# Kernel tuning notes

Hardware: AMD Instinct MI355X
Metric: run time of the kernel (lower is better)

The kernel has to match this reference:

```python
import jax, jax.numpy as jnp
import numpy as np

B, S, H, NH = 16, 1024, 512, 8
DH = H // NH
EPS = 1e-12
COV_MIN = 1e-24


def _split_heads(x):
    b, s, _ = x.shape
    return x.reshape(b, s, NH, DH).transpose(0, 2, 1, 3)  # [B,NH,S,DH]


def _merge_heads(x):
    b, nh, s, dh = x.shape
    return x.transpose(0, 2, 1, 3).reshape(b, s, nh * dh)


def _layernorm(x, w, b):
    u = jnp.mean(x, -1, keepdims=True)
    s = jnp.mean((x - u) ** 2, -1, keepdims=True)
    return w * ((x - u) / jnp.sqrt(s + EPS)) + b


def _wasserstein(mq, cq, mk, ck):
    # mean part: ||mq_i - mk_j||^2 via matmul expansion
    ret = (-2.0 * jnp.einsum('bhid,bhjd->bhij', mq, mk)
           + jnp.sum(mq ** 2, -1)[..., :, None]
           + jnp.sum(mk ** 2, -1)[..., None, :])
    sq_cq = jnp.sqrt(jnp.clip(cq, COV_MIN))
    sq_ck = jnp.sqrt(jnp.clip(ck, COV_MIN))
    cov_ret = (-2.0 * jnp.einsum('bhid,bhjd->bhij', sq_cq, sq_ck)
               + jnp.sum(cq, -1)[..., :, None]
               + jnp.sum(ck, -1)[..., None, :])
    return ret + cov_ret


def setup_inputs() -> dict:
    key = jax.random.key(0)
    ks = jax.random.split(key, 16)
    d = {
        'x_mean': jax.random.normal(ks[0], (B, S, H), jnp.float32),
        'x_resp_mean': jax.random.normal(ks[1], (B, S, H), jnp.float32),
        'x_cov': jax.random.normal(ks[2], (B, S, H), jnp.float32),
        'x_resp_cov': jax.random.normal(ks[3], (B, S, H), jnp.float32),
    }
    causal = jnp.tril(jnp.ones((S, S), bool))
    d['attn_mask'] = jnp.where(causal, 0.0, -1e4).astype(jnp.float32)[None, None]
    names = ['mq', 'mk', 'mv', 'cq', 'ck', 'cv', 'md', 'cd']
    for i, n in enumerate(names):
        d[n + '_w'] = jax.random.normal(ks[4 + i], (H, H), jnp.float32) * 0.02
        d[n + '_b'] = jnp.zeros((H,), jnp.float32)
    d['ln_w'] = jnp.ones((H,), jnp.float32)
    d['ln_b'] = jnp.zeros((H,), jnp.float32)
    return d


def reference(x_mean, x_resp_mean, x_cov, x_resp_cov, attn_mask,
              mq_w, mq_b, mk_w, mk_b, mv_w, mv_b,
              cq_w, cq_b, ck_w, ck_b, cv_w, cv_b,
              md_w, md_b, cd_w, cd_b, ln_w, ln_b):
    mq = _split_heads(x_mean @ mq_w + mq_b)
    mk = _split_heads(x_mean @ mk_w + mk_b)
    mv = _split_heads(x_resp_mean @ mv_w + mv_b)
    cq = _split_heads(jax.nn.elu(x_cov @ cq_w + cq_b) + 1.0)
    ck = _split_heads(jax.nn.elu(x_cov @ ck_w + ck_b) + 1.0)
    cv = _split_heads(jax.nn.elu(x_resp_cov @ cv_w + cv_b) + 1.0)

    scores = -_wasserstein(mq, cq, mk, ck) / np.sqrt(DH).astype(np.float32)
    scores = scores + attn_mask
    probs = jax.nn.softmax(scores, axis=-1)  # [B,NH,S,S]
    # zero_pad=True: zero out the first query row
    probs = probs.at[:, :, 0, :].set(0.0)

    mean_ctx = _merge_heads(jnp.einsum('bhij,bhjd->bhid', probs, mv))
    cov_ctx = _merge_heads(jnp.einsum('bhij,bhjd->bhid', probs ** 2, cv))

    mean_h = _layernorm(mean_ctx @ md_w + md_b + x_mean, ln_w, ln_b)
    cov_h = _layernorm(cov_ctx @ cd_w + cd_b + x_cov, ln_w, ln_b)
    return mean_h, cov_h, probs
```

## Files before the change

kernel.cpp:

```cpp
#include <hip/hip_runtime.h>
#include <math.h>

#define SLEN 1024
#define NH 8
#define DH 64
#define HDIM 512
#define BATCH 16
#define NROWS (BATCH * SLEN)
#define BHN (BATCH * NH)
#define BHROWS (BHN * SLEN)

typedef short bf16x8 __attribute__((ext_vector_type(8)));
typedef unsigned short u16x8 __attribute__((ext_vector_type(8)));
typedef float f32x4 __attribute__((ext_vector_type(4)));

__device__ __forceinline__ unsigned short f2bf(float f) {
    unsigned u = __float_as_uint(f);
    u += 0x7fffu + ((u >> 16) & 1u);
    return (unsigned short)(u >> 16);
}
__device__ __forceinline__ float bf2f(unsigned short h) {
    return __uint_as_float(((unsigned)h) << 16);
}

struct Args {
    const float *xm, *xrm, *xc, *xrc;
    const float *w[8], *bias[8];
    const float *ln_w, *ln_b;
    unsigned short *xbf, *wt;
    float *sums;
    unsigned short *qcat, *kcat, *vcat, *vcat_t, *ctxm, *ctxc;
    float *out_m, *out_c, *probs;
};

__global__ void __launch_bounds__(256) cvt_inputs_k(Args P) {
    const int which = blockIdx.y;
    const float *s = which == 0 ? P.xm : which == 1 ? P.xrm : which == 2 ? P.xc : P.xrc;
    unsigned short *d = P.xbf + (size_t)which * 8388608;
    const long long i = ((long long)blockIdx.x * 256 + threadIdx.x) * 8;
    if (i >= 8388608) return;
    float4 a = *(const float4 *)(s + i);
    float4 b = *(const float4 *)(s + i + 4);
    u16x8 o;
    o[0] = f2bf(a.x); o[1] = f2bf(a.y); o[2] = f2bf(a.z); o[3] = f2bf(a.w);
    o[4] = f2bf(b.x); o[5] = f2bf(b.y); o[6] = f2bf(b.z); o[7] = f2bf(b.w);
    *(u16x8 *)(d + i) = o;
}

__global__ void __launch_bounds__(256) wtrans_k(Args P) {
    const int op = blockIdx.y;
    const float *W = P.w[op];
    unsigned short *WT = P.wt + (size_t)op * 262144;
    const int kt = blockIdx.x >> 3, nt = blockIdx.x & 7;
    __shared__ float Ws[64][65];
    const int t = threadIdx.x;
#pragma unroll
    for (int it = 0; it < 4; ++it) {
        int g = t + 256 * it;
        int k = g >> 4, n4 = (g & 15) * 4;
        float4 v = *(const float4 *)(W + (size_t)(kt * 64 + k) * 512 + nt * 64 + n4);
        Ws[k][n4] = v.x; Ws[k][n4 + 1] = v.y; Ws[k][n4 + 2] = v.z; Ws[k][n4 + 3] = v.w;
    }
    __syncthreads();
#pragma unroll
    for (int it = 0; it < 2; ++it) {
        int g = t + 256 * it;
        int n = g >> 3, kg = (g & 7) * 8;
        u16x8 o;
#pragma unroll
        for (int e = 0; e < 8; ++e) o[e] = f2bf(Ws[kg + e][n]);
        *(u16x8 *)(WT + (size_t)(nt * 64 + n) * 512 + kt * 64 + kg) = o;
    }
}

__global__ void __launch_bounds__(256) mgemm0_k(Args P) {
    const int op = blockIdx.z;
    const int srcidx[6] = {0, 0, 1, 2, 2, 3};
    const unsigned short *Abf = P.xbf + (size_t)srcidx[op] * 8388608;
    const unsigned short *WT = P.wt + (size_t)op * 262144;
    const float *bias = P.bias[op];
    unsigned short *dstb; int doff, act;
    switch (op) {
        case 0: dstb = P.qcat; doff = 0;  act = 0; break;
        case 1: dstb = P.kcat; doff = 0;  act = 0; break;
        case 2: dstb = P.vcat; doff = 0;  act = 0; break;
        case 3: dstb = P.qcat; doff = 64; act = 1; break;
        case 4: dstb = P.kcat; doff = 64; act = 1; break;
        default:dstb = P.vcat; doff = 64; act = 2; break;
    }
    const int lin = blockIdx.y * 4 + blockIdx.x;
    const int xcd = lin & 7, idx = lin >> 3;
    const int m0 = (xcd * 16 + (idx >> 2)) * 128;
    const int n0 = (idx & 3) * 128;

    __shared__ unsigned short As[128][64];
    __shared__ unsigned short Bs[128][64];
    const int t = threadIdx.x;
    const int wid = t >> 6, lane = t & 63;
    const int wm = wid >> 1, wn = wid & 1;
    const int l16 = lane & 15, lq = lane >> 4;

    f32x4 acc[4][4];
#pragma unroll
    for (int i = 0; i < 4; ++i)
#pragma unroll
        for (int j = 0; j < 4; ++j) acc[i][j] = (f32x4)(0.f);

    for (int k0 = 0; k0 < 512; k0 += 64) {
        __syncthreads();
#pragma unroll
        for (int it = 0; it < 4; ++it) {
            int g = t + 256 * it;
            int r = g >> 3, cg = g & 7;
            bf16x8 av = *(const bf16x8 *)(Abf + (size_t)(m0 + r) * 512 + k0 + cg * 8);
            *(bf16x8 *)&As[r][(cg ^ (r & 7)) * 8] = av;
            bf16x8 bv = *(const bf16x8 *)(WT + (size_t)(n0 + r) * 512 + k0 + cg * 8);
            *(bf16x8 *)&Bs[r][(cg ^ (r & 7)) * 8] = bv;
        }
        __syncthreads();
#pragma unroll
        for (int kk = 0; kk < 2; ++kk) {
            bf16x8 a[4], b[4];
#pragma unroll
            for (int mf = 0; mf < 4; ++mf) {
                int r = wm * 64 + mf * 16 + l16;
                int cg = kk * 4 + lq;
                a[mf] = *(const bf16x8 *)&As[r][(cg ^ (r & 7)) * 8];
            }
#pragma unroll
            for (int nf = 0; nf < 4; ++nf) {
                int r = wn * 64 + nf * 16 + l16;
                int cg = kk * 4 + lq;
                b[nf] = *(const bf16x8 *)&Bs[r][(cg ^ (r & 7)) * 8];
            }
#pragma unroll
            for (int mf = 0; mf < 4; ++mf)
#pragma unroll
                for (int nf = 0; nf < 4; ++nf)
                    acc[mf][nf] = __builtin_amdgcn_mfma_f32_16x16x32_bf16(a[mf], b[nf], acc[mf][nf], 0, 0, 0);
        }
    }

#pragma unroll
    for (int mf = 0; mf < 4; ++mf) {
#pragma unroll
        for (int nf = 0; nf < 4; ++nf) {
#pragma unroll
            for (int r = 0; r < 4; ++r) {
                const int i = m0 + wm * 64 + mf * 16 + lq * 4 + r;
                const int j = n0 + wn * 64 + nf * 16 + l16;
                float v = acc[mf][nf][r] + bias[j];
                if (act == 1) {
                    float e = v > 0.f ? v + 1.f : expf(v);
                    v = sqrtf(fmaxf(e, 1e-24f));
                } else if (act == 2) {
                    v = v > 0.f ? v + 1.f : expf(v);
                }
                const int b_ = i >> 10, s_ = i & (SLEN - 1);
                const int h_ = j >> 6, d_ = j & (DH - 1);
                dstb[((size_t)(b_ * NH + h_) * SLEN + s_) * 128 + doff + d_] = f2bf(v);
            }
        }
    }
}

__global__ void __launch_bounds__(256) vtrans_k(Args P) {
    const int bh = blockIdx.y;
    const int s0 = blockIdx.x * 128;
    __shared__ unsigned short Ts[128][136];
    const unsigned short *src = P.vcat + (size_t)bh * SLEN * 128;
    unsigned short *dst = P.vcat_t + (size_t)bh * 128 * SLEN;
    const int t = threadIdx.x;
#pragma unroll
    for (int it = 0; it < 8; ++it) {
        int g = t + 256 * it;
        int s = g >> 4, dg = g & 15;
        *(u16x8 *)&Ts[s][dg * 8] = *(const u16x8 *)(src + (size_t)(s0 + s) * 128 + dg * 8);
    }
    __syncthreads();
#pragma unroll
    for (int it = 0; it < 8; ++it) {
        int g = t + 256 * it;
        int d = g >> 4, sg = g & 15;
        u16x8 o;
#pragma unroll
        for (int e = 0; e < 8; ++e) o[e] = Ts[sg * 8 + e][d];
        *(u16x8 *)(dst + (size_t)d * SLEN + s0 + sg * 8) = o;
    }
}

__global__ void __launch_bounds__(256) rowsum_k(Args P) {
    const int t = threadIdx.x;
    const int wv = t >> 6, lane = t & 63;
    const long long row = (long long)blockIdx.x * 4 + wv;
    const unsigned short *src = (row < BHROWS) ? P.qcat : P.kcat;
    const long long r = row & (BHROWS - 1);
    const unsigned short *p = src + r * 128;
    float a = bf2f(p[lane]), b = bf2f(p[64 + lane]);
    float v = a * a + b * b;
#pragma unroll
    for (int o = 32; o > 0; o >>= 1) v += __shfl_xor(v, o);
    if (lane == 0) P.sums[row] = v;
}

__global__ void __launch_bounds__(512, 4) flash_k(Args P) {
    const int bh = blockIdx.x;
    const int qt = 31 - (int)blockIdx.y;
    const int q0 = qt * 32;
    __shared__ unsigned short Ep[32][1024];
    __shared__ unsigned short Ks[64][128];
    unsigned short (*Vt)[64] = reinterpret_cast<unsigned short (*)[64]>(&Ks[0][0]);
    float *scr = reinterpret_cast<float *>(&Ks[0][0]);

    const int t = threadIdx.x;
    const int w = t >> 6, lane = t & 63;
    const int l16 = lane & 15, lq = lane >> 4;
    const int mg = w >> 2, q4 = w & 3;

    const unsigned short *qc = P.qcat + (size_t)bh * SLEN * 128;
    const unsigned short *kc = P.kcat + (size_t)bh * SLEN * 128;
    const float *qsum = P.sums + (size_t)bh * SLEN;
    const float *ksum = P.sums + BHROWS + (size_t)bh * SLEN;
    float *pout = P.probs + ((size_t)bh * SLEN + q0) * SLEN;

    const unsigned short *qrow = qc + (size_t)(q0 + mg * 16 + l16) * 128;
    bf16x8 qfr[4];
#pragma unroll
    for (int kk = 0; kk < 4; ++kk) qfr[kk] = *(const bf16x8 *)(qrow + (kk * 4 + lq) * 8);
    float qs[4];
#pragma unroll
    for (int r = 0; r < 4; ++r) qs[r] = qsum[q0 + mg * 16 + lq * 4 + r];

    const int nkt = (q0 >> 6) + 1;
    const int rK = q4 * 16 + l16;
    float tpart[4] = {0.f, 0.f, 0.f, 0.f};

    const int sr0 = t >> 4, sg = t & 15;
    const int sr1 = sr0 + 32;
    bf16x8 kreg0 = *(const bf16x8 *)(kc + (size_t)sr0 * 128 + sg * 8);
    bf16x8 kreg1 = *(const bf16x8 *)(kc + (size_t)sr1 * 128 + sg * 8);
    float ksreg = ksum[rK];

    for (int kt = 0; kt < nkt; ++kt) {
        __syncthreads();
        *(bf16x8 *)&Ks[sr0][(sg ^ (sr0 & 7)) * 8] = kreg0;
        *(bf16x8 *)&Ks[sr1][(sg ^ (sr1 & 7)) * 8] = kreg1;
        if (kt + 1 < nkt) {
            kreg0 = *(const bf16x8 *)(kc + (size_t)((kt + 1) * 64 + sr0) * 128 + sg * 8);
            kreg1 = *(const bf16x8 *)(kc + (size_t)((kt + 1) * 64 + sr1) * 128 + sg * 8);
        }
        __syncthreads();

        const float ksv = ksreg;
        if (kt + 1 < nkt) ksreg = ksum[(kt + 1) * 64 + rK];

        f32x4 acc = (f32x4)(0.f);
#pragma unroll
        for (int kk = 0; kk < 4; ++kk) {
            bf16x8 b = *(const bf16x8 *)&Ks[rK][((kk * 4 + lq) ^ (rK & 7)) * 8];
            acc = __builtin_amdgcn_mfma_f32_16x16x32_bf16(qfr[kk], b, acc, 0, 0, 0);
        }
        const int j = kt * 64 + rK;
#pragma unroll
        for (int r = 0; r < 4; ++r) {
            const int row = mg * 16 + lq * 4 + r;
            const int i = q0 + row;
            float sv = (2.f * acc[r] - qs[r] - ksv) * 0.125f;
            float e = (j <= i) ? __expf(sv) : 0.f;
            tpart[r] += e;
            Ep[row][(((j >> 3) ^ (row & 7)) << 3) | (j & 7)] = f2bf(e);
        }
    }

    {
        const int zrow = t >> 4;
        f32x4 z = (f32x4)(0.f);
        for (int c4 = nkt * 16 + (t & 15); c4 < 256; c4 += 16)
            *(f32x4 *)(pout + (size_t)zrow * SLEN + c4 * 4) = z;
    }

#pragma unroll
    for (int o = 1; o < 16; o <<= 1)
#pragma unroll
        for (int r = 0; r < 4; ++r) tpart[r] += __shfl_xor(tpart[r], o);
    __syncthreads();
    if (l16 == 0) {
#pragma unroll
        for (int r = 0; r < 4; ++r) scr[q4 * 32 + mg * 16 + lq * 4 + r] = tpart[r];
    }
    __syncthreads();
    float invP;
    {
        const int row = t >> 4;
        const float T = scr[row] + scr[32 + row] + scr[64 + row] + scr[96 + row];
        invP = (q0 + row == 0) ? 0.f : (1.f / T);
    }
    float invC[4];
#pragma unroll
    for (int r = 0; r < 4; ++r) {
        const int row = mg * 16 + lq * 4 + r;
        const float T = scr[row] + scr[32 + row] + scr[64 + row] + scr[96 + row];
        invC[r] = (q0 + row == 0) ? 0.f : (1.f / T);
    }
    __syncthreads();

    const int cov = q4 >> 1;
    f32x4 pacc[2];
    pacc[0] = (f32x4)(0.f); pacc[1] = (f32x4)(0.f);
    const unsigned short *vtg = P.vcat_t + (size_t)bh * 128 * SLEN;
    const int vr0 = t >> 3, vg = t & 7;
    const int vr1 = vr0 + 64;
    bf16x8 vreg0 = *(const bf16x8 *)(vtg + (size_t)vr0 * SLEN + vg * 8);
    bf16x8 vreg1 = *(const bf16x8 *)(vtg + (size_t)vr1 * SLEN + vg * 8);

    for (int kt = 0; kt < nkt; ++kt) {
        __syncthreads();
        *(bf16x8 *)&Vt[vr0][(vg ^ (vr0 & 7)) * 8] = vreg0;
        *(bf16x8 *)&Vt[vr1][(vg ^ (vr1 & 7)) * 8] = vreg1;
        if (kt + 1 < nkt) {
            vreg0 = *(const bf16x8 *)(vtg + (size_t)vr0 * SLEN + (kt + 1) * 64 + vg * 8);
            vreg1 = *(const bf16x8 *)(vtg + (size_t)vr1 * SLEN + (kt + 1) * 64 + vg * 8);
        }
        __syncthreads();

#pragma unroll
        for (int kk = 0; kk < 2; ++kk) {
            const int row = mg * 16 + l16;
            const int gg = (kt * 8) + kk * 4 + lq;
            bf16x8 af = *(const bf16x8 *)&Ep[row][((gg ^ (row & 7)) << 3)];
            if (cov) {
                u16x8 u = (u16x8)af, sq;
#pragma unroll
                for (int e = 0; e < 8; ++e) {
                    float f = bf2f(u[e]);
                    sq[e] = f2bf(f * f);
                }
                af = (bf16x8)sq;
            }
#pragma unroll
            for (int nf = 0; nf < 2; ++nf) {
                const int d = q4 * 32 + nf * 16 + l16;
                bf16x8 bf = *(const bf16x8 *)&Vt[d][((kk * 4 + lq) ^ (d & 7)) * 8];
                pacc[nf] = __builtin_amdgcn_mfma_f32_16x16x32_bf16(af, bf, pacc[nf], 0, 0, 0);
            }
        }

        {
            const int prow = t >> 4, slot = t & 15;
            const int col = kt * 64 + slot * 4;
            const int g = col >> 3, o4 = (slot & 1) * 4;
            u16x8 v = *(const u16x8 *)&Ep[prow][((g ^ (prow & 7)) << 3)];
            f32x4 ov;
            if (kt == nkt - 1) {
                const int i = q0 + prow;
#pragma unroll
                for (int e = 0; e < 4; ++e)
                    ov[e] = (col + e <= i) ? bf2f(v[o4 + e]) * invP : 0.f;
            } else {
#pragma unroll
                for (int e = 0; e < 4; ++e)
                    ov[e] = bf2f(v[o4 + e]) * invP;
            }
            *(f32x4 *)(pout + (size_t)prow * SLEN + col) = ov;
        }
    }

    unsigned short *dst = cov ? P.ctxc : P.ctxm;
    const int b_ = bh >> 3, h_ = bh & 7;
#pragma unroll
    for (int nf = 0; nf < 2; ++nf) {
#pragma unroll
        for (int r = 0; r < 4; ++r) {
            const int row = mg * 16 + lq * 4 + r;
            const int s_ = q0 + row;
            const float scale = cov ? invC[r] * invC[r] : invC[r];
            dst[((size_t)b_ * SLEN + s_) * HDIM + h_ * 64 + (q4 & 1) * 32 + nf * 16 + l16] =
                f2bf(pacc[nf][r] * scale);
        }
    }
}

__global__ void __launch_bounds__(512, 4) mgemm_ln_k(Args P) {
    const int op = blockIdx.y;
    const unsigned short *Abf = op ? P.ctxc : P.ctxm;
    const unsigned short *WT = P.wt + (size_t)(6 + op) * 262144;
    const float *bias = P.bias[6 + op];
    const float *resid = op ? P.xc : P.xm;
    float *out = op ? P.out_c : P.out_m;
    const int m0 = blockIdx.x * 64;

    __shared__ unsigned short As[64][64];
    __shared__ unsigned short Bs[512][64];
    __shared__ float Red[64][4][2];

    const int t = threadIdx.x;
    const int w = t >> 6, lane = t & 63;
    const int wm = w >> 2, wn = w & 3;
    const int l16 = lane & 15, lq = lane >> 4;

    f32x4 acc[2][8];
#pragma unroll
    for (int mf = 0; mf < 2; ++mf)
#pragma unroll
        for (int nf = 0; nf < 8; ++nf) acc[mf][nf] = (f32x4)(0.f);

    for (int k0 = 0; k0 < 512; k0 += 64) {
        __syncthreads();
        {
            int r = t >> 3, cg = t & 7;
            *(bf16x8 *)&As[r][(cg ^ (r & 7)) * 8] =
                *(const bf16x8 *)(Abf + (size_t)(m0 + r) * 512 + k0 + cg * 8);
        }
#pragma unroll
        for (int it = 0; it < 8; ++it) {
            int g = t + 512 * it;
            int r = g >> 3, cg = g & 7;
            *(bf16x8 *)&Bs[r][(cg ^ (r & 7)) * 8] =
                *(const bf16x8 *)(WT + (size_t)r * 512 + k0 + cg * 8);
        }
        __syncthreads();
#pragma unroll
        for (int kk = 0; kk < 2; ++kk) {
            bf16x8 a[2];
#pragma unroll
            for (int mf = 0; mf < 2; ++mf) {
                int r = wm * 32 + mf * 16 + l16;
                a[mf] = *(const bf16x8 *)&As[r][((kk * 4 + lq) ^ (r & 7)) * 8];
            }
#pragma unroll
            for (int nf = 0; nf < 8; ++nf) {
                int rn = wn * 128 + nf * 16 + l16;
                bf16x8 b = *(const bf16x8 *)&Bs[rn][((kk * 4 + lq) ^ (rn & 7)) * 8];
#pragma unroll
                for (int mf = 0; mf < 2; ++mf)
                    acc[mf][nf] = __builtin_amdgcn_mfma_f32_16x16x32_bf16(a[mf], b, acc[mf][nf], 0, 0, 0);
            }
        }
    }

    float bv[8];
#pragma unroll
    for (int nf = 0; nf < 8; ++nf) bv[nf] = bias[wn * 128 + nf * 16 + l16];

    float s0[2][4], s1[2][4];
#pragma unroll
    for (int mf = 0; mf < 2; ++mf)
#pragma unroll
        for (int r = 0; r < 4; ++r) { s0[mf][r] = 0.f; s1[mf][r] = 0.f; }

#pragma unroll
    for (int mf = 0; mf < 2; ++mf) {
#pragma unroll
        for (int r = 0; r < 4; ++r) {
            const int i = m0 + wm * 32 + mf * 16 + lq * 4 + r;
            const float *rrow = resid + (size_t)i * HDIM + wn * 128 + l16;
#pragma unroll
            for (int nf = 0; nf < 8; ++nf) {
                float x = acc[mf][nf][r] + bv[nf] + rrow[nf * 16];
                acc[mf][nf][r] = x;
                s0[mf][r] += x;
                s1[mf][r] += x * x;
            }
        }
    }
#pragma unroll
    for (int o = 1; o < 16; o <<= 1)
#pragma unroll
        for (int mf = 0; mf < 2; ++mf)
#pragma unroll
            for (int r = 0; r < 4; ++r) {
                s0[mf][r] += __shfl_xor(s0[mf][r], o);
                s1[mf][r] += __shfl_xor(s1[mf][r], o);
            }
    if (l16 == 0) {
#pragma unroll
        for (int mf = 0; mf < 2; ++mf)
#pragma unroll
            for (int r = 0; r < 4; ++r) {
                const int row = wm * 32 + mf * 16 + lq * 4 + r;
                Red[row][wn][0] = s0[mf][r];
                Red[row][wn][1] = s1[mf][r];
            }
    }
    __syncthreads();

    float lnw[8], lnb[8];
#pragma unroll
    for (int nf = 0; nf < 8; ++nf) {
        const int j = wn * 128 + nf * 16 + l16;
        lnw[nf] = P.ln_w[j]; lnb[nf] = P.ln_b[j];
    }
#pragma unroll
    for (int mf = 0; mf < 2; ++mf) {
#pragma unroll
        for (int r = 0; r < 4; ++r) {
            const int row = wm * 32 + mf * 16 + lq * 4 + r;
            const int i = m0 + row;
            const float S  = Red[row][0][0] + Red[row][1][0] + Red[row][2][0] + Red[row][3][0];
            const float SS = Red[row][0][1] + Red[row][1][1] + Red[row][2][1] + Red[row][3][1];
            const float mean = S * (1.f / 512.f);
            const float var = SS * (1.f / 512.f) - mean * mean;
            const float inv = 1.f / sqrtf(var + 1e-12f);
            float *orow = out + (size_t)i * HDIM + wn * 128 + l16;
#pragma unroll
            for (int nf = 0; nf < 8; ++nf)
                orow[nf * 16] = lnw[nf] * ((acc[mf][nf][r] - mean) * inv) + lnb[nf];
        }
    }
}

extern "C" void kernel_launch(void *const *d_in, const int *in_sizes, int n_in,
                              void *d_out, int out_size, void *d_ws, size_t ws_size,
                              hipStream_t stream) {
    (void)in_sizes; (void)n_in; (void)out_size; (void)ws_size;
    Args P;
    P.xm  = (const float *)d_in[0];
    P.xrm = (const float *)d_in[1];
    P.xc  = (const float *)d_in[2];
    P.xrc = (const float *)d_in[3];
    for (int i = 0; i < 8; ++i) {
        P.w[i]    = (const float *)d_in[5 + 2 * i];
        P.bias[i] = (const float *)d_in[6 + 2 * i];
    }
    P.ln_w = (const float *)d_in[21];
    P.ln_b = (const float *)d_in[22];

    char *ws = (char *)d_ws;
    P.xbf    = (unsigned short *)(ws);
    P.vcat_t = (unsigned short *)(ws);
    P.ctxm   = (unsigned short *)(ws + 33554432);
    P.ctxc   = (unsigned short *)(ws + 50331648);
    P.wt     = (unsigned short *)(ws + 67108864);
    P.sums   = (float *)(ws + 71303168);
    P.qcat   = (unsigned short *)(ws + 72351744);
    P.kcat   = (unsigned short *)(ws + 105906176);
    P.vcat   = (unsigned short *)(ws + 139460608);

    P.out_m = (float *)d_out;
    P.out_c = (float *)d_out + 8388608;
    P.probs = (float *)d_out + 16777216;

    cvt_inputs_k<<<dim3(4096, 4), dim3(256), 0, stream>>>(P);
    wtrans_k<<<dim3(64, 8), dim3(256), 0, stream>>>(P);
    mgemm0_k<<<dim3(4, 128, 6), dim3(256), 0, stream>>>(P);
    vtrans_k<<<dim3(8, 128), dim3(256), 0, stream>>>(P);
    rowsum_k<<<dim3(65536), dim3(256), 0, stream>>>(P);
    flash_k<<<dim3(128, 32), dim3(512), 0, stream>>>(P);
    mgemm_ln_k<<<dim3(256, 2), dim3(512), 0, stream>>>(P);
}
```

Before: 479.3 us.

## Use direct global-to-LDS loads in GEMMs, exp2 softmax, and MFMA priority hints

Replaces register-staged global→LDS copies in the projection GEMM and the output GEMM+LayerNorm kernel with global_load_lds DMA-style loads. The XOR swizzle moves from the LDS store address to the global read address, so the LDS layout is unchanged. In attention it folds the 1/8 scale and log2(e) into one constant and calls exp2f, and it wraps the MFMA sections in s_setprio to favour matrix issue across waves. The aim is to cut VGPR traffic and the cost of the exponential. The risk is correctness if the per-wave LDS offsets do not match the lane layout that the direct-load instruction assumes.

```diff
diff --git a/kernel.cpp b/kernel.cpp
--- a/kernel.cpp
+++ b/kernel.cpp
@@ -21,6 +21,13 @@
 }
 __device__ __forceinline__ float bf2f(unsigned short h) {
     return __uint_as_float(((unsigned)h) << 16);
+}
+
+__device__ __forceinline__ void gload16(const void *g, void *l) {
+    __builtin_amdgcn_global_load_lds(
+        (const __attribute__((address_space(1))) unsigned int *)g,
+        (__attribute__((address_space(3))) unsigned int *)l,
+        16, 0, 0);
 }
 
 struct Args {
@@ -99,6 +106,8 @@
     const int wid = t >> 6, lane = t & 63;
     const int wm = wid >> 1, wn = wid & 1;
     const int l16 = lane & 15, lq = lane >> 4;
+    char *AsB = (char *)&As[0][0];
+    char *BsB = (char *)&Bs[0][0];
 
     f32x4 acc[4][4];
 #pragma unroll
@@ -112,10 +121,9 @@
         for (int it = 0; it < 4; ++it) {
             int g = t + 256 * it;
             int r = g >> 3, cg = g & 7;
-            bf16x8 av = *(const bf16x8 *)(Abf + (size_t)(m0 + r) * 512 + k0 + cg * 8);
-            *(bf16x8 *)&As[r][(cg ^ (r & 7)) * 8] = av;
-            bf16x8 bv = *(const bf16x8 *)(WT + (size_t)(n0 + r) * 512 + k0 + cg * 8);
-            *(bf16x8 *)&Bs[r][(cg ^ (r & 7)) * 8] = bv;
+            int sc = (cg ^ (r & 7)) * 8;
+            gload16(Abf + (size_t)(m0 + r) * 512 + k0 + sc, AsB + it * 4096 + wid * 1024);
+            gload16(WT + (size_t)(n0 + r) * 512 + k0 + sc, BsB + it * 4096 + wid * 1024);
         }
         __syncthreads();
 #pragma unroll
@@ -234,6 +242,7 @@
     const int nkt = (q0 >> 6) + 1;
     const int rK = q4 * 16 + l16;
     float tpart[4] = {0.f, 0.f, 0.f, 0.f};
+    const float C = 0.18033688f;
 
     const int sr0 = t >> 4, sg = t & 15;
     const int sr1 = sr0 + 32;
@@ -254,19 +263,21 @@
         const float ksv = ksreg;
         if (kt + 1 < nkt) ksreg = ksum[(kt + 1) * 64 + rK];
 
+        __builtin_amdgcn_s_setprio(1);
         f32x4 acc = (f32x4)(0.f);
 #pragma unroll
         for (int kk = 0; kk < 4; ++kk) {
             bf16x8 b = *(const bf16x8 *)&Ks[rK][((kk * 4 + lq) ^ (rK & 7)) * 8];
             acc = __builtin_amdgcn_mfma_f32_16x16x32_bf16(qfr[kk], b, acc, 0, 0, 0);
         }
+        __builtin_amdgcn_s_setprio(0);
         const int j = kt * 64 + rK;
 #pragma unroll
         for (int r = 0; r < 4; ++r) {
             const int row = mg * 16 + lq * 4 + r;
             const int i = q0 + row;
-            float sv = (2.f * acc[r] - qs[r] - ksv) * 0.125f;
-            float e = (j <= i) ? __expf(sv) : 0.f;
+            float sv = (2.f * acc[r] - qs[r] - ksv) * C;
+            float e = (j <= i) ? exp2f(sv) : 0.f;
             tpart[r] += e;
             Ep[row][(((j >> 3) ^ (row & 7)) << 3) | (j & 7)] = f2bf(e);
         }
@@ -323,6 +334,7 @@
         }
         __syncthreads();
 
+        __builtin_amdgcn_s_setprio(1);
 #pragma unroll
         for (int kk = 0; kk < 2; ++kk) {
             const int row = mg * 16 + l16;
@@ -344,6 +356,7 @@
                 pacc[nf] = __builtin_amdgcn_mfma_f32_16x16x32_bf16(af, bf, pacc[nf], 0, 0, 0);
             }
         }
+        __builtin_amdgcn_s_setprio(0);
 
         {
             const int prow = t >> 4, slot = t & 15;
@@ -397,6 +410,8 @@
     const int w = t >> 6, lane = t & 63;
     const int wm = w >> 2, wn = w & 3;
     const int l16 = lane & 15, lq = lane >> 4;
+    char *AsB = (char *)&As[0][0];
+    char *BsB = (char *)&Bs[0][0];
 
     f32x4 acc[2][8];
 #pragma unroll
@@ -408,15 +423,15 @@
         __syncthreads();
         {
             int r = t >> 3, cg = t & 7;
-            *(bf16x8 *)&As[r][(cg ^ (r & 7)) * 8] =
-                *(const bf16x8 *)(Abf + (size_t)(m0 + r) * 512 + k0 + cg * 8);
+            int sc = (cg ^ (r & 7)) * 8;
+            gload16(Abf + (size_t)(m0 + r) * 512 + k0 + sc, AsB + w * 1024);
         }
 #pragma unroll
         for (int it = 0; it < 8; ++it) {
             int g = t + 512 * it;
             int r = g >> 3, cg = g & 7;
-            *(bf16x8 *)&Bs[r][(cg ^ (r & 7)) * 8] =
-                *(const bf16x8 *)(WT + (size_t)r * 512 + k0 + cg * 8);
+            int sc = (cg ^ (r & 7)) * 8;
+            gload16(WT + (size_t)r * 512 + k0 + sc, BsB + it * 8192 + w * 1024);
         }
         __syncthreads();
 #pragma unroll
```

Result: faster. 466.5 us (-2.7%).
